# Performance work log

Measured on AMD Instinct MI355X. Metric: run time of the kernel, lower is better.

## Reference

```python
import jax, jax.numpy as jnp
import numpy as np

N_HEAD = 16
N_KV_HEAD = 4


def setup_inputs() -> dict:
    key = jax.random.key(0)
    ks = jax.random.split(key, 5)
    B, T, D = 2, 2048, 2048
    kdim = D // N_HEAD  # 128
    s = 0.02
    x = jax.random.normal(ks[0], (B, T, D), dtype=jnp.float32)
    Wq = jax.random.normal(ks[1], (D, D), dtype=jnp.float32) * s
    Wk = jax.random.normal(ks[2], (D, N_KV_HEAD * kdim), dtype=jnp.float32) * s
    Wv = jax.random.normal(ks[3], (D, N_KV_HEAD * kdim), dtype=jnp.float32) * s
    Wo = jax.random.normal(ks[4], (D, D), dtype=jnp.float32) * s
    return {"x": x, "Wq": Wq, "Wk": Wk, "Wv": Wv, "Wo": Wo}


def reference(x, Wq, Wk, Wv, Wo):
    B, T, D = x.shape
    h, kv = N_HEAD, N_KV_HEAD
    g = h // kv  # query groups per kv head
    kdim = D // h
    Q = (x @ Wq).reshape(B, T, h, kdim).transpose(0, 2, 1, 3)   # [B,h,T,k]
    K = (x @ Wk).reshape(B, T, kv, kdim).transpose(0, 2, 1, 3)  # [B,kv,T,k]
    V = (x @ Wv).reshape(B, T, kv, kdim).transpose(0, 2, 1, 3)
    # repeat_interleave(g, dim=1): kv outer, group inner
    K = jnp.broadcast_to(K[:, :, None], (B, kv, g, T, kdim)).reshape(B, h, T, kdim)
    V = jnp.broadcast_to(V[:, :, None], (B, kv, g, T, kdim)).reshape(B, h, T, kdim)
    scores = jnp.einsum('bhqd,bhkd->bhqk', Q, K) / jnp.sqrt(jnp.float32(kdim))
    causal = jnp.tril(jnp.ones((T, T), dtype=bool))
    scores = jnp.where(causal[None, None], scores, jnp.float32(-jnp.inf))
    A = jax.nn.softmax(scores, axis=-1)
    Y = jnp.einsum('bhqk,bhkd->bhqd', A, V).transpose(0, 2, 1, 3).reshape(B, T, D)
    return Y @ Wo
```

## Files before the change

### kernel.cpp

```cpp
#include <hip/hip_runtime.h>
#include <hip/hip_bf16.h>

typedef __bf16 bf16x8 __attribute__((ext_vector_type(8)));
typedef float f32x4 __attribute__((ext_vector_type(4)));

__device__ __forceinline__ unsigned short f2bf(float f) {
  unsigned int u = __float_as_uint(f);
  u += 0x7fffu + ((u >> 16) & 1u);
  return (unsigned short)(u >> 16);
}

__device__ __forceinline__ unsigned int pack2(float lo, float hi) {
  __hip_bfloat162 h = __float22bfloat162_rn(float2{lo, hi});
  return *(unsigned int*)&h;
}

__device__ __forceinline__ void load_lds16(const void* g, void* l) {
  __builtin_amdgcn_global_load_lds(
      (const __attribute__((address_space(1))) unsigned int*)g,
      (__attribute__((address_space(3))) unsigned int*)l, 16, 0, 0);
}

__global__ void cvt_x(const float* __restrict__ in, unsigned short* __restrict__ out) {
  size_t i = ((size_t)blockIdx.x * 256 + threadIdx.x) * 4;
  float4 v = *(const float4*)(in + i);
  ushort4 o;
  o.x = f2bf(v.x); o.y = f2bf(v.y); o.z = f2bf(v.z); o.w = f2bf(v.w);
  *(ushort4*)(out + i) = o;
}

__global__ void tr_w(const float* __restrict__ in, unsigned short* __restrict__ out,
                     int ldin, int ldout) {
  __shared__ float tile[32][33];
  const int c0 = blockIdx.x * 32, r0 = blockIdx.y * 32;
  const int tx = threadIdx.x, ty = threadIdx.y;
#pragma unroll
  for (int j = 0; j < 4; ++j)
    tile[ty + j * 8][tx] = in[(size_t)(r0 + ty + j * 8) * ldin + c0 + tx];
  __syncthreads();
#pragma unroll
  for (int j = 0; j < 4; ++j)
    out[(size_t)(c0 + ty + j * 8) * ldout + r0 + tx] = f2bf(tile[tx][ty + j * 8]);
}

__global__ void tr_v(const unsigned short* __restrict__ QKV, unsigned short* __restrict__ VT) {
  __shared__ unsigned short tile[32][33];
  const int z = blockIdx.z, b = z >> 2, kvh = z & 3;
  const unsigned short* in = QKV + (size_t)(b * 2048) * 3072 + 2560 + kvh * 128;
  unsigned short* out = VT + (size_t)z * 128 * 2048;
  const int c0 = blockIdx.x * 32, r0 = blockIdx.y * 32;
  const int tx = threadIdx.x, ty = threadIdx.y;
#pragma unroll
  for (int j = 0; j < 4; ++j)
    tile[ty + j * 8][tx] = in[(size_t)(r0 + ty + j * 8) * 3072 + c0 + tx];
  __syncthreads();
#pragma unroll
  for (int j = 0; j < 4; ++j)
    out[(size_t)(c0 + ty + j * 8) * 2048 + r0 + tx] = tile[tx][ty + j * 8];
}

template <int OUTF32>
__global__ void gemm_bt(const unsigned short* __restrict__ A,
                        const unsigned short* __restrict__ B,
                        void* __restrict__ Cv, int M, int N, int K) {
  __shared__ __attribute__((aligned(16))) unsigned short As[128 * 64];
  __shared__ __attribute__((aligned(16))) unsigned short Bs[128 * 64];
  const int tid = threadIdx.x;
  const int lane = tid & 63;
  const int cl = lane & 15, rg = lane >> 4;
  const int wave = tid >> 6;
  const int bm = blockIdx.y, bn = blockIdx.x;
  const int wm = wave >> 1, wn = wave & 1;
  f32x4 acc[4][4] = {};
  const int nk = K >> 6;
  for (int kt = 0; kt < nk; ++kt) {
    const int k0 = kt << 6;
    __syncthreads();
#pragma unroll
    for (int i = 0; i < 8; ++i) {
      const int Ls = (i & 3) * 256 + tid;
      const int r = Ls >> 3, s = Ls & 7;
      const int c = s ^ (r & 7);
      const unsigned short* src;
      unsigned short* dst;
      if (i < 4) {
        src = A + (size_t)(bm * 128 + r) * K + k0 + c * 8;
        dst = As + (((i & 3) * 256 + (tid & 0xC0)) << 3);
      } else {
        src = B + (size_t)(bn * 128 + r) * K + k0 + c * 8;
        dst = Bs + (((i & 3) * 256 + (tid & 0xC0)) << 3);
      }
      load_lds16(src, dst);
    }
    __syncthreads();
#pragma unroll
    for (int ks = 0; ks < 2; ++ks) {
      bf16x8 af[4], bfr[4];
#pragma unroll
      for (int m = 0; m < 4; ++m) {
        const int row = wm * 64 + m * 16 + cl;
        const int p = (ks * 4 + rg) ^ (row & 7);
        af[m] = *(const bf16x8*)(As + row * 64 + p * 8);
      }
#pragma unroll
      for (int n = 0; n < 4; ++n) {
        const int row = wn * 64 + n * 16 + cl;
        const int p = (ks * 4 + rg) ^ (row & 7);
        bfr[n] = *(const bf16x8*)(Bs + row * 64 + p * 8);
      }
#pragma unroll
      for (int m = 0; m < 4; ++m)
#pragma unroll
        for (int n = 0; n < 4; ++n)
          acc[m][n] = __builtin_amdgcn_mfma_f32_16x16x32_bf16(af[m], bfr[n], acc[m][n], 0, 0, 0);
    }
  }
#pragma unroll
  for (int m = 0; m < 4; ++m)
#pragma unroll
    for (int n = 0; n < 4; ++n)
#pragma unroll
      for (int i = 0; i < 4; ++i) {
        const int row = bm * 128 + wm * 64 + m * 16 + rg * 4 + i;
        const int col = bn * 128 + wn * 64 + n * 16 + cl;
        if (OUTF32)
          ((float*)Cv)[(size_t)row * N + col] = acc[m][n][i];
        else
          ((unsigned short*)Cv)[(size_t)row * N + col] = f2bf(acc[m][n][i]);
      }
}

__global__ __launch_bounds__(256, 2) void attn(const unsigned short* __restrict__ QKV,
                                               const unsigned short* __restrict__ VT,
                                               unsigned short* __restrict__ O) {
  __shared__ __attribute__((aligned(16))) unsigned short Ks[2][64 * 128];
  __shared__ __attribute__((aligned(16))) unsigned short VTs[2][128 * 64];
  const int T = 2048, LD = 3072, D = 2048;
  const int jp = blockIdx.x, h = blockIdx.y, b = blockIdx.z;
  const int kvh = h >> 2;
  const int tid = threadIdx.x, lane = tid & 63, wave = tid >> 6;
  const int cl = lane & 15, rg = lane >> 4;
  const bool abit = (lane & 16) != 0, bbit = (lane & 32) != 0;
  const bool ab = abit != bbit;
  const unsigned short* Kbase = QKV + (size_t)b * T * LD + 2048 + kvh * 128;
  const unsigned short* Vbase = VT + (size_t)(b * 4 + kvh) * 128 * T;

  auto stage = [&](int sb, int k0) {
#pragma unroll
    for (int i = 0; i < 4; ++i) {
      const int Ls = i * 256 + tid;
      const int r = Ls >> 4, s = Ls & 15, c = s ^ (r & 7);
      load_lds16(Kbase + (size_t)(k0 + r) * LD + c * 8,
                 &Ks[sb][(i * 256 + (tid & 0xC0)) * 8]);
    }
#pragma unroll
    for (int i = 0; i < 4; ++i) {
      const int Ls = i * 256 + tid;
      const int r = Ls >> 3, s = Ls & 7, c = s ^ (r & 7);
      load_lds16(Vbase + (size_t)r * T + k0 + c * 8,
                 &VTs[sb][(i * 256 + (tid & 0xC0)) * 8]);
    }
  };

  const float scale = 0.08838834764831845f;

#pragma unroll 1
  for (int pass = 0; pass < 2; ++pass) {
    const int jt = pass ? (31 - jp) : jp;
    const int q0 = jt * 64;
    const int nkt = jt + 1;
    const int qrow = q0 + wave * 16 + cl;

    const unsigned short* Qp = QKV + (size_t)(b * T + qrow) * LD + h * 128;
    bf16x8 qf[4];
#pragma unroll
    for (int ks = 0; ks < 4; ++ks) qf[ks] = *(const bf16x8*)(Qp + ks * 32 + rg * 8);

    f32x4 o[8] = {};
    float m = -1e30f, l = 0.f;
    int buf = 0;

    stage(0, 0);
    __syncthreads();

#pragma unroll 1
    for (int kt = 0; kt < nkt; ++kt) {
      if (kt + 1 < nkt) stage(buf ^ 1, (kt + 1) * 64);

      f32x4 sa[4] = {};
      __builtin_amdgcn_s_setprio(1);
#pragma unroll
      for (int ks = 0; ks < 4; ++ks) {
#pragma unroll
        for (int n = 0; n < 4; ++n) {
          const int row = n * 16 + cl;
          const int p = (ks * 4 + rg) ^ (row & 7);
          const bf16x8 kf = *(const bf16x8*)(&Ks[buf][row * 128 + p * 8]);
          sa[n] = __builtin_amdgcn_mfma_f32_16x16x32_bf16(kf, qf[ks], sa[n], 0, 0, 0);
        }
      }
      __builtin_amdgcn_s_setprio(0);

      const int k0 = kt * 64;
      float p[4][4];
      float pmax = -1e30f;
      if (kt == jt) {
#pragma unroll
        for (int n = 0; n < 4; ++n)
#pragma unroll
          for (int i = 0; i < 4; ++i) {
            const int kg = k0 + n * 16 + rg * 4 + i;
            p[n][i] = (kg > qrow) ? -1e30f : sa[n][i] * scale;
            pmax = fmaxf(pmax, p[n][i]);
          }
      } else {
#pragma unroll
        for (int n = 0; n < 4; ++n)
#pragma unroll
          for (int i = 0; i < 4; ++i) {
            p[n][i] = sa[n][i] * scale;
            pmax = fmaxf(pmax, p[n][i]);
          }
      }
      pmax = fmaxf(pmax, __shfl_xor(pmax, 16));
      pmax = fmaxf(pmax, __shfl_xor(pmax, 32));

      if (!__all(pmax <= m + 8.f)) {
        const float mnew = fmaxf(m, pmax);
        const float alpha = __expf(m - mnew);
        m = mnew;
        l *= alpha;
#pragma unroll
        for (int n2 = 0; n2 < 8; ++n2) o[n2] *= alpha;
      }

      float rs = 0.f;
#pragma unroll
      for (int n = 0; n < 4; ++n)
#pragma unroll
        for (int i = 0; i < 4; ++i) {
          p[n][i] = __expf(p[n][i] - m);
          rs += p[n][i];
        }
      rs += __shfl_xor(rs, 16);
      rs += __shfl_xor(rs, 32);
      l += rs;

      unsigned int F[2][4];
#pragma unroll
      for (int ks2 = 0; ks2 < 2; ++ks2) {
        const unsigned int pk00 = pack2(p[2 * ks2][0], p[2 * ks2][1]);
        const unsigned int pk01 = pack2(p[2 * ks2][2], p[2 * ks2][3]);
        const unsigned int pk10 = pack2(p[2 * ks2 + 1][0], p[2 * ks2 + 1][1]);
        const unsigned int pk11 = pack2(p[2 * ks2 + 1][2], p[2 * ks2 + 1][3]);
        const unsigned int s0 = bbit ? pk00 : pk10;
        const unsigned int s1 = bbit ? pk01 : pk11;
        const unsigned int r0 = (unsigned int)__shfl_xor((int)s0, 32);
        const unsigned int r1 = (unsigned int)__shfl_xor((int)s1, 32);
        const unsigned int gk0 = bbit ? pk10 : pk00;
        const unsigned int gk1 = bbit ? pk11 : pk01;
        const unsigned int t0 = ab ? gk0 : r0;
        const unsigned int t1 = ab ? gk1 : r1;
        const unsigned int u0 = (unsigned int)__shfl_xor((int)t0, 16);
        const unsigned int u1 = (unsigned int)__shfl_xor((int)t1, 16);
        const unsigned int k20 = ab ? r0 : gk0;
        const unsigned int k21 = ab ? r1 : gk1;
        F[ks2][0] = abit ? u0 : k20;
        F[ks2][1] = abit ? u1 : k21;
        F[ks2][2] = abit ? k20 : u0;
        F[ks2][3] = abit ? k21 : u1;
      }

      __builtin_amdgcn_s_setprio(1);
#pragma unroll
      for (int ks2 = 0; ks2 < 2; ++ks2) {
        uint4 fu = make_uint4(F[ks2][0], F[ks2][1], F[ks2][2], F[ks2][3]);
        const bf16x8 pf = *(const bf16x8*)&fu;
#pragma unroll
        for (int n2 = 0; n2 < 8; ++n2) {
          const int dr = n2 * 16 + cl;
          const int p2 = (ks2 * 4 + rg) ^ (dr & 7);
          const bf16x8 vf = *(const bf16x8*)(&VTs[buf][dr * 64 + p2 * 8]);
          o[n2] = __builtin_amdgcn_mfma_f32_16x16x32_bf16(vf, pf, o[n2], 0, 0, 0);
        }
      }
      __builtin_amdgcn_s_setprio(0);

      __syncthreads();
      buf ^= 1;
    }

    const float rl = __builtin_amdgcn_rcpf(l);
#pragma unroll
    for (int n2 = 0; n2 < 8; ++n2) {
      ushort4 ov;
      ov.x = f2bf(o[n2][0] * rl);
      ov.y = f2bf(o[n2][1] * rl);
      ov.z = f2bf(o[n2][2] * rl);
      ov.w = f2bf(o[n2][3] * rl);
      *(ushort4*)(O + (size_t)(b * T + qrow) * D + h * 128 + n2 * 16 + rg * 4) = ov;
    }
  }
}

extern "C" void kernel_launch(void* const* d_in, const int* in_sizes, int n_in,
                              void* d_out, int out_size, void* d_ws, size_t ws_size,
                              hipStream_t stream) {
  const float* x = (const float*)d_in[0];
  const float* Wq = (const float*)d_in[1];
  const float* Wk = (const float*)d_in[2];
  const float* Wv = (const float*)d_in[3];
  const float* Wo = (const float*)d_in[4];
  float* out = (float*)d_out;

  char* ws = (char*)d_ws;
  unsigned short* xb    = (unsigned short*)(ws);
  unsigned short* WqkvT = (unsigned short*)(ws + 16777216);
  unsigned short* WoT   = (unsigned short*)(ws + 29360128);
  unsigned short* QKV   = (unsigned short*)(ws + 37748736);
  unsigned short* VTb   = (unsigned short*)(ws + 62914560);

  cvt_x<<<dim3(8192), dim3(256), 0, stream>>>(x, xb);
  tr_w<<<dim3(64, 64), dim3(32, 8), 0, stream>>>(Wq, WqkvT, 2048, 2048);
  tr_w<<<dim3(16, 64), dim3(32, 8), 0, stream>>>(Wk, WqkvT + (size_t)2048 * 2048, 512, 2048);
  tr_w<<<dim3(16, 64), dim3(32, 8), 0, stream>>>(Wv, WqkvT + (size_t)2560 * 2048, 512, 2048);
  tr_w<<<dim3(64, 64), dim3(32, 8), 0, stream>>>(Wo, WoT, 2048, 2048);

  gemm_bt<0><<<dim3(24, 32), dim3(256), 0, stream>>>(xb, WqkvT, QKV, 4096, 3072, 2048);
  tr_v<<<dim3(4, 64, 8), dim3(32, 8), 0, stream>>>(QKV, VTb);
  attn<<<dim3(16, 16, 2), dim3(256), 0, stream>>>(QKV, VTb, xb);
  gemm_bt<1><<<dim3(16, 32), dim3(256), 0, stream>>>(xb, WoT, out, 4096, 2048, 2048);
}
```

Measured before the change: 201.1 us.

## Use 128-row query tiles per attention block instead of paired 64-row passes

The attention kernel now gives each block one 128-row query tile, with each wave handling two 16-row sub-tiles, instead of two balanced 64-row passes. Each K/V tile staged in LDS now feeds twice as many MFMAs, which halves LDS staging and global K/V traffic per query. The cost is uneven work across blocks: the largest tile needs 32 K tiles at double the compute. The old per-block balance from pairing tiles is gone, and the first waves compute some fully masked diagonal tiles. Register pressure also rises from the doubled accumulators.

After: 229.8 us. 1.14x slower.

```diff
diff --git a/kernel.cpp b/kernel.cpp
--- a/kernel.cpp
+++ b/kernel.cpp
@@ -136,7 +136,8 @@
   __shared__ __attribute__((aligned(16))) unsigned short Ks[2][64 * 128];
   __shared__ __attribute__((aligned(16))) unsigned short VTs[2][128 * 64];
   const int T = 2048, LD = 3072, D = 2048;
-  const int jp = blockIdx.x, h = blockIdx.y, b = blockIdx.z;
+  const int jt = 15 - blockIdx.x;
+  const int h = blockIdx.y, b = blockIdx.z;
   const int kvh = h >> 2;
   const int tid = threadIdx.x, lane = tid & 63, wave = tid >> 6;
   const int cl = lane & 15, rg = lane >> 4;
@@ -163,75 +164,81 @@
   };
 
   const float scale = 0.08838834764831845f;
+  const int q0 = jt * 128;
+  const int nkt = 2 * jt + 2;
+  const int qb = q0 + wave * 32;
+
+  bf16x8 qf[2][4];
+#pragma unroll
+  for (int sub = 0; sub < 2; ++sub) {
+    const unsigned short* Qp = QKV + (size_t)(b * T + qb + sub * 16 + cl) * LD + h * 128;
+#pragma unroll
+    for (int ks = 0; ks < 4; ++ks) qf[sub][ks] = *(const bf16x8*)(Qp + ks * 32 + rg * 8);
+  }
+
+  f32x4 o[2][8] = {};
+  float mrun[2] = {-1e30f, -1e30f}, lrun[2] = {0.f, 0.f};
+  int buf = 0;
+
+  stage(0, 0);
+  __syncthreads();
 
 #pragma unroll 1
-  for (int pass = 0; pass < 2; ++pass) {
-    const int jt = pass ? (31 - jp) : jp;
-    const int q0 = jt * 64;
-    const int nkt = jt + 1;
-    const int qrow = q0 + wave * 16 + cl;
-
-    const unsigned short* Qp = QKV + (size_t)(b * T + qrow) * LD + h * 128;
-    bf16x8 qf[4];
-#pragma unroll
-    for (int ks = 0; ks < 4; ++ks) qf[ks] = *(const bf16x8*)(Qp + ks * 32 + rg * 8);
-
-    f32x4 o[8] = {};
-    float m = -1e30f, l = 0.f;
-    int buf = 0;
-
-    stage(0, 0);
-    __syncthreads();
-
-#pragma unroll 1
-    for (int kt = 0; kt < nkt; ++kt) {
-      if (kt + 1 < nkt) stage(buf ^ 1, (kt + 1) * 64);
-
-      f32x4 sa[4] = {};
-      __builtin_amdgcn_s_setprio(1);
-#pragma unroll
-      for (int ks = 0; ks < 4; ++ks) {
-#pragma unroll
-        for (int n = 0; n < 4; ++n) {
-          const int row = n * 16 + cl;
-          const int p = (ks * 4 + rg) ^ (row & 7);
-          const bf16x8 kf = *(const bf16x8*)(&Ks[buf][row * 128 + p * 8]);
-          sa[n] = __builtin_amdgcn_mfma_f32_16x16x32_bf16(kf, qf[ks], sa[n], 0, 0, 0);
-        }
-      }
-      __builtin_amdgcn_s_setprio(0);
-
-      const int k0 = kt * 64;
-      float p[4][4];
+  for (int kt = 0; kt < nkt; ++kt) {
+    if (kt + 1 < nkt) stage(buf ^ 1, (kt + 1) * 64);
+
+    f32x4 sa[2][4] = {};
+    __builtin_amdgcn_s_setprio(1);
+#pragma unroll
+    for (int ks = 0; ks < 4; ++ks) {
+#pragma unroll
+      for (int n = 0; n < 4; ++n) {
+        const int row = n * 16 + cl;
+        const int p = (ks * 4 + rg) ^ (row & 7);
+        const bf16x8 kf = *(const bf16x8*)(&Ks[buf][row * 128 + p * 8]);
+        sa[0][n] = __builtin_amdgcn_mfma_f32_16x16x32_bf16(kf, qf[0][ks], sa[0][n], 0, 0, 0);
+        sa[1][n] = __builtin_amdgcn_mfma_f32_16x16x32_bf16(kf, qf[1][ks], sa[1][n], 0, 0, 0);
+      }
+    }
+    __builtin_amdgcn_s_setprio(0);
+
+    const int k0 = kt * 64;
+    float p[2][4][4];
+    unsigned int F[2][2][4];
+
+#pragma unroll
+    for (int sub = 0; sub < 2; ++sub) {
+      const int qbs = qb + sub * 16;
+      const int qrow = qbs + cl;
       float pmax = -1e30f;
-      if (kt == jt) {
+      if (k0 + 63 > qbs) {
 #pragma unroll
         for (int n = 0; n < 4; ++n)
 #pragma unroll
           for (int i = 0; i < 4; ++i) {
             const int kg = k0 + n * 16 + rg * 4 + i;
-            p[n][i] = (kg > qrow) ? -1e30f : sa[n][i] * scale;
-            pmax = fmaxf(pmax, p[n][i]);
+            p[sub][n][i] = (kg > qrow) ? -1e30f : sa[sub][n][i] * scale;
+            pmax = fmaxf(pmax, p[sub][n][i]);
           }
       } else {
 #pragma unroll
         for (int n = 0; n < 4; ++n)
 #pragma unroll
           for (int i = 0; i < 4; ++i) {
-            p[n][i] = sa[n][i] * scale;
-            pmax = fmaxf(pmax, p[n][i]);
+            p[sub][n][i] = sa[sub][n][i] * scale;
+            pmax = fmaxf(pmax, p[sub][n][i]);
           }
       }
       pmax = fmaxf(pmax, __shfl_xor(pmax, 16));
       pmax = fmaxf(pmax, __shfl_xor(pmax, 32));
 
-      if (!__all(pmax <= m + 8.f)) {
-        const float mnew = fmaxf(m, pmax);
-        const float alpha = __expf(m - mnew);
-        m = mnew;
-        l *= alpha;
-#pragma unroll
-        for (int n2 = 0; n2 < 8; ++n2) o[n2] *= alpha;
+      if (!__all(pmax <= mrun[sub] + 8.f)) {
+        const float mnew = fmaxf(mrun[sub], pmax);
+        const float alpha = __expf(mrun[sub] - mnew);
+        mrun[sub] = mnew;
+        lrun[sub] *= alpha;
+#pragma unroll
+        for (int n2 = 0; n2 < 8; ++n2) o[sub][n2] *= alpha;
       }
 
       float rs = 0.f;
@@ -239,20 +246,19 @@
       for (int n = 0; n < 4; ++n)
 #pragma unroll
         for (int i = 0; i < 4; ++i) {
-          p[n][i] = __expf(p[n][i] - m);
-          rs += p[n][i];
+          p[sub][n][i] = __expf(p[sub][n][i] - mrun[sub]);
+          rs += p[sub][n][i];
         }
       rs += __shfl_xor(rs, 16);
       rs += __shfl_xor(rs, 32);
-      l += rs;
-
-      unsigned int F[2][4];
+      lrun[sub] += rs;
+
 #pragma unroll
       for (int ks2 = 0; ks2 < 2; ++ks2) {
-        const unsigned int pk00 = pack2(p[2 * ks2][0], p[2 * ks2][1]);
-        const unsigned int pk01 = pack2(p[2 * ks2][2], p[2 * ks2][3]);
-        const unsigned int pk10 = pack2(p[2 * ks2 + 1][0], p[2 * ks2 + 1][1]);
-        const unsigned int pk11 = pack2(p[2 * ks2 + 1][2], p[2 * ks2 + 1][3]);
+        const unsigned int pk00 = pack2(p[sub][2 * ks2][0], p[sub][2 * ks2][1]);
+        const unsigned int pk01 = pack2(p[sub][2 * ks2][2], p[sub][2 * ks2][3]);
+        const unsigned int pk10 = pack2(p[sub][2 * ks2 + 1][0], p[sub][2 * ks2 + 1][1]);
+        const unsigned int pk11 = pack2(p[sub][2 * ks2 + 1][2], p[sub][2 * ks2 + 1][3]);
         const unsigned int s0 = bbit ? pk00 : pk10;
         const unsigned int s1 = bbit ? pk01 : pk11;
         const unsigned int r0 = (unsigned int)__shfl_xor((int)s0, 32);
@@ -265,39 +271,46 @@
         const unsigned int u1 = (unsigned int)__shfl_xor((int)t1, 16);
         const unsigned int k20 = ab ? r0 : gk0;
         const unsigned int k21 = ab ? r1 : gk1;
-        F[ks2][0] = abit ? u0 : k20;
-        F[ks2][1] = abit ? u1 : k21;
-        F[ks2][2] = abit ? k20 : u0;
-        F[ks2][3] = abit ? k21 : u1;
-      }
-
-      __builtin_amdgcn_s_setprio(1);
-#pragma unroll
-      for (int ks2 = 0; ks2 < 2; ++ks2) {
-        uint4 fu = make_uint4(F[ks2][0], F[ks2][1], F[ks2][2], F[ks2][3]);
-        const bf16x8 pf = *(const bf16x8*)&fu;
-#pragma unroll
-        for (int n2 = 0; n2 < 8; ++n2) {
-          const int dr = n2 * 16 + cl;
-          const int p2 = (ks2 * 4 + rg) ^ (dr & 7);
-          const bf16x8 vf = *(const bf16x8*)(&VTs[buf][dr * 64 + p2 * 8]);
-          o[n2] = __builtin_amdgcn_mfma_f32_16x16x32_bf16(vf, pf, o[n2], 0, 0, 0);
-        }
-      }
-      __builtin_amdgcn_s_setprio(0);
-
-      __syncthreads();
-      buf ^= 1;
-    }
-
-    const float rl = __builtin_amdgcn_rcpf(l);
+        F[sub][ks2][0] = abit ? u0 : k20;
+        F[sub][ks2][1] = abit ? u1 : k21;
+        F[sub][ks2][2] = abit ? k20 : u0;
+        F[sub][ks2][3] = abit ? k21 : u1;
+      }
+    }
+
+    __builtin_amdgcn_s_setprio(1);
+#pragma unroll
+    for (int ks2 = 0; ks2 < 2; ++ks2) {
+      uint4 f0 = make_uint4(F[0][ks2][0], F[0][ks2][1], F[0][ks2][2], F[0][ks2][3]);
+      uint4 f1 = make_uint4(F[1][ks2][0], F[1][ks2][1], F[1][ks2][2], F[1][ks2][3]);
+      const bf16x8 pf0 = *(const bf16x8*)&f0;
+      const bf16x8 pf1 = *(const bf16x8*)&f1;
+#pragma unroll
+      for (int n2 = 0; n2 < 8; ++n2) {
+        const int dr = n2 * 16 + cl;
+        const int p2 = (ks2 * 4 + rg) ^ (dr & 7);
+        const bf16x8 vf = *(const bf16x8*)(&VTs[buf][dr * 64 + p2 * 8]);
+        o[0][n2] = __builtin_amdgcn_mfma_f32_16x16x32_bf16(vf, pf0, o[0][n2], 0, 0, 0);
+        o[1][n2] = __builtin_amdgcn_mfma_f32_16x16x32_bf16(vf, pf1, o[1][n2], 0, 0, 0);
+      }
+    }
+    __builtin_amdgcn_s_setprio(0);
+
+    __syncthreads();
+    buf ^= 1;
+  }
+
+#pragma unroll
+  for (int sub = 0; sub < 2; ++sub) {
+    const int qrow = qb + sub * 16 + cl;
+    const float rl = __builtin_amdgcn_rcpf(lrun[sub]);
 #pragma unroll
     for (int n2 = 0; n2 < 8; ++n2) {
       ushort4 ov;
-      ov.x = f2bf(o[n2][0] * rl);
-      ov.y = f2bf(o[n2][1] * rl);
-      ov.z = f2bf(o[n2][2] * rl);
-      ov.w = f2bf(o[n2][3] * rl);
+      ov.x = f2bf(o[sub][n2][0] * rl);
+      ov.y = f2bf(o[sub][n2][1] * rl);
+      ov.z = f2bf(o[sub][n2][2] * rl);
+      ov.w = f2bf(o[sub][n2][3] * rl);
       *(ushort4*)(O + (size_t)(b * T + qrow) * D + h * 128 + n2 * 16 + rg * 4) = ov;
     }
   }
```

## Use 256x256-tile 8-wave pipelined GEMM for QKV projection

Applied to the files above, without the earlier changes.

Adds a new GEMM kernel with 256x256 output tiles, 512 threads, and double-buffered LDS staged in K halves through direct global-to-LDS loads. Loads for the next k-tile are interleaved with MFMA phases, and it uses swizzled LDS, explicit waitcnt and barriers, and raised wave priority around the MFMA blocks. It replaces the 128x128 GEMM for the QKV projection to get more data reuse per tile and overlap memory with compute. In exchange the grid drops to 192 blocks, which may underfill a 256-CU device, and the kernel has heavy register pressure from 128 accumulator floats per thread.

Result: no change. 197.9 us (-1.6%).

```diff
diff --git a/kernel.cpp b/kernel.cpp
--- a/kernel.cpp
+++ b/kernel.cpp
@@ -127,6 +127,153 @@
           ((float*)Cv)[(size_t)row * N + col] = acc[m][n][i];
         else
           ((unsigned short*)Cv)[(size_t)row * N + col] = f2bf(acc[m][n][i]);
+      }
+}
+
+template <int OUTF32>
+__global__ __launch_bounds__(512, 2) void gemm256(const unsigned short* __restrict__ A,
+                                                  const unsigned short* __restrict__ B,
+                                                  void* __restrict__ Cv, int M, int N, int K) {
+  __shared__ __attribute__((aligned(16))) unsigned short lds[2][2][2][256 * 32];
+  const int tid = threadIdx.x;
+  const int lane = tid & 63;
+  const int cl = lane & 15, rg = lane >> 4;
+  const int wave = tid >> 6;
+  const int wm = wave >> 2, wn = wave & 3;
+  const int bm = blockIdx.y, bn = blockIdx.x;
+  const int NK = K >> 6;
+  const int rowA = bm * 256, rowB = bn * 256;
+
+  f32x4 acc[8][4] = {};
+
+  auto stage_half = [&](int buf, int op, int h, const unsigned short* Mat, int rb, int kt) {
+#pragma unroll
+    for (int i = 0; i < 2; ++i) {
+      const int L = i * 512 + tid;
+      const int r = L >> 2;
+      const int c = (L & 3) ^ ((r >> 1) & 3);
+      const unsigned short* src = Mat + (size_t)(rb + r) * K + kt * 64 + h * 32 + c * 8;
+      load_lds16(src, (void*)(&lds[buf][op][h][0] + (size_t)(i * 512 + (tid & ~63)) * 8));
+    }
+  };
+
+  stage_half(0, 0, 0, A, rowA, 0);
+  stage_half(0, 1, 0, B, rowB, 0);
+  stage_half(0, 0, 1, A, rowA, 0);
+  stage_half(0, 1, 1, B, rowB, 0);
+  asm volatile("s_waitcnt vmcnt(4)" ::: "memory");
+  __builtin_amdgcn_s_barrier();
+
+  int buf = 0;
+#pragma unroll 1
+  for (int kt = 0; kt < NK; ++kt) {
+    const bool nl = (kt + 1 < NK);
+    bf16x8 af[4], bfr[4];
+
+#pragma unroll
+    for (int f = 0; f < 4; ++f) {
+      const int r = 128 * wm + 16 * f + cl;
+      af[f] = *(const bf16x8*)(&lds[buf][0][0][(r * 4 + (rg ^ ((r >> 1) & 3))) * 8]);
+    }
+#pragma unroll
+    for (int nf = 0; nf < 4; ++nf) {
+      const int r = 64 * wn + 16 * nf + cl;
+      bfr[nf] = *(const bf16x8*)(&lds[buf][1][0][(r * 4 + (rg ^ ((r >> 1) & 3))) * 8]);
+    }
+    if (nl) stage_half(buf ^ 1, 0, 0, A, rowA, kt + 1);
+    __builtin_amdgcn_sched_barrier(0);
+    __builtin_amdgcn_s_barrier();
+    asm volatile("s_waitcnt lgkmcnt(0)" ::: "memory");
+    __builtin_amdgcn_sched_barrier(0);
+    __builtin_amdgcn_s_setprio(1);
+#pragma unroll
+    for (int f = 0; f < 4; ++f)
+#pragma unroll
+      for (int nf = 0; nf < 4; ++nf)
+        acc[f][nf] = __builtin_amdgcn_mfma_f32_16x16x32_bf16(af[f], bfr[nf], acc[f][nf], 0, 0, 0);
+    __builtin_amdgcn_s_setprio(0);
+    __builtin_amdgcn_s_barrier();
+
+#pragma unroll
+    for (int f = 0; f < 4; ++f) {
+      const int r = 128 * wm + 16 * (f + 4) + cl;
+      af[f] = *(const bf16x8*)(&lds[buf][0][0][(r * 4 + (rg ^ ((r >> 1) & 3))) * 8]);
+    }
+    if (nl) stage_half(buf ^ 1, 1, 0, B, rowB, kt + 1);
+    __builtin_amdgcn_sched_barrier(0);
+    __builtin_amdgcn_s_barrier();
+    asm volatile("s_waitcnt lgkmcnt(0)" ::: "memory");
+    __builtin_amdgcn_sched_barrier(0);
+    __builtin_amdgcn_s_setprio(1);
+#pragma unroll
+    for (int f = 0; f < 4; ++f)
+#pragma unroll
+      for (int nf = 0; nf < 4; ++nf)
+        acc[f + 4][nf] = __builtin_amdgcn_mfma_f32_16x16x32_bf16(af[f], bfr[nf], acc[f + 4][nf], 0, 0, 0);
+    __builtin_amdgcn_s_setprio(0);
+    if (nl) asm volatile("s_waitcnt vmcnt(4)" ::: "memory");
+    else    asm volatile("s_waitcnt vmcnt(0)" ::: "memory");
+    __builtin_amdgcn_s_barrier();
+
+#pragma unroll
+    for (int f = 0; f < 4; ++f) {
+      const int r = 128 * wm + 16 * f + cl;
+      af[f] = *(const bf16x8*)(&lds[buf][0][1][(r * 4 + (rg ^ ((r >> 1) & 3))) * 8]);
+    }
+#pragma unroll
+    for (int nf = 0; nf < 4; ++nf) {
+      const int r = 64 * wn + 16 * nf + cl;
+      bfr[nf] = *(const bf16x8*)(&lds[buf][1][1][(r * 4 + (rg ^ ((r >> 1) & 3))) * 8]);
+    }
+    if (nl) stage_half(buf ^ 1, 0, 1, A, rowA, kt + 1);
+    __builtin_amdgcn_sched_barrier(0);
+    __builtin_amdgcn_s_barrier();
+    asm volatile("s_waitcnt lgkmcnt(0)" ::: "memory");
+    __builtin_amdgcn_sched_barrier(0);
+    __builtin_amdgcn_s_setprio(1);
+#pragma unroll
+    for (int f = 0; f < 4; ++f)
+#pragma unroll
+      for (int nf = 0; nf < 4; ++nf)
+        acc[f][nf] = __builtin_amdgcn_mfma_f32_16x16x32_bf16(af[f], bfr[nf], acc[f][nf], 0, 0, 0);
+    __builtin_amdgcn_s_setprio(0);
+    __builtin_amdgcn_s_barrier();
+
+#pragma unroll
+    for (int f = 0; f < 4; ++f) {
+      const int r = 128 * wm + 16 * (f + 4) + cl;
+      af[f] = *(const bf16x8*)(&lds[buf][0][1][(r * 4 + (rg ^ ((r >> 1) & 3))) * 8]);
+    }
+    if (nl) stage_half(buf ^ 1, 1, 1, B, rowB, kt + 1);
+    __builtin_amdgcn_sched_barrier(0);
+    __builtin_amdgcn_s_barrier();
+    asm volatile("s_waitcnt lgkmcnt(0)" ::: "memory");
+    __builtin_amdgcn_sched_barrier(0);
+    __builtin_amdgcn_s_setprio(1);
+#pragma unroll
+    for (int f = 0; f < 4; ++f)
+#pragma unroll
+      for (int nf = 0; nf < 4; ++nf)
+        acc[f + 4][nf] = __builtin_amdgcn_mfma_f32_16x16x32_bf16(af[f], bfr[nf], acc[f + 4][nf], 0, 0, 0);
+    __builtin_amdgcn_s_setprio(0);
+    if (nl) asm volatile("s_waitcnt vmcnt(4)" ::: "memory");
+    __builtin_amdgcn_s_barrier();
+
+    buf ^= 1;
+  }
+
+#pragma unroll
+  for (int f = 0; f < 8; ++f)
+#pragma unroll
+    for (int nf = 0; nf < 4; ++nf)
+#pragma unroll
+      for (int i = 0; i < 4; ++i) {
+        const int row = bm * 256 + wm * 128 + f * 16 + rg * 4 + i;
+        const int col = bn * 256 + wn * 64 + nf * 16 + cl;
+        if (OUTF32)
+          ((float*)Cv)[(size_t)row * N + col] = acc[f][nf][i];
+        else
+          ((unsigned short*)Cv)[(size_t)row * N + col] = f2bf(acc[f][nf][i]);
       }
 }
 
@@ -326,7 +473,7 @@
   tr_w<<<dim3(16, 64), dim3(32, 8), 0, stream>>>(Wv, WqkvT + (size_t)2560 * 2048, 512, 2048);
   tr_w<<<dim3(64, 64), dim3(32, 8), 0, stream>>>(Wo, WoT, 2048, 2048);
 
-  gemm_bt<0><<<dim3(24, 32), dim3(256), 0, stream>>>(xb, WqkvT, QKV, 4096, 3072, 2048);
+  gemm256<0><<<dim3(12, 16), dim3(512), 0, stream>>>(xb, WqkvT, QKV, 4096, 3072, 2048);
   tr_v<<<dim3(4, 64, 8), dim3(32, 8), 0, stream>>>(QKV, VTb);
   attn<<<dim3(16, 16, 2), dim3(256), 0, stream>>>(QKV, VTb, xb);
   gemm_bt<1><<<dim3(16, 32), dim3(256), 0, stream>>>(xb, WoT, out, 4096, 2048, 2048);
```
